# Kernel optimization log

Measured on AMD Instinct MI355X. Metric: run time of the kernel, lower is better.

## Reference

```python
import jax, jax.numpy as jnp
import numpy as np


def setup_inputs() -> dict:
    key = jax.random.key(0)
    k1, k2, k3 = jax.random.split(key, 3)
    B, K, C, H, W = 8, 8, 256, 64, 64
    return {
        "IR_features": jax.random.normal(k1, (B, K, C, H, W), dtype=jnp.float32),
        "CR_features": jax.random.normal(k2, (B, K, C, H, W), dtype=jnp.float32),
        "CT_feature": jax.random.normal(k3, (B, C, H, W), dtype=jnp.float32),
    }


def reference(IR_features, CR_features, CT_feature):
    # sim: [B, K, C, 1, 1] = <CT, CR>_{HW} / ||CR||_{HW}
    dot = jnp.sum(CT_feature[:, None] * CR_features, axis=(3, 4), keepdims=True)
    norm = jnp.sqrt(jnp.sum(CR_features ** 2, axis=(3, 4), keepdims=True))
    sim = dot / norm
    weights = jax.nn.softmax(sim * 2.0, axis=1)  # softmax over K styles
    # style feature: weighted sum over K -> [B, C, H, W]
    style_feature = jnp.sum(IR_features * weights, axis=1)
    return style_feature
```

## Files before the change

### kernel.cpp

```cpp
#include <hip/hip_runtime.h>
#include <math.h>

#define B_DIM 8
#define K_DIM 8
#define C_DIM 256
#define HW4   1024
#define CHUNK 4

__global__ __launch_bounds__(256)
void dfs_mixer_fused(const float4* __restrict__ IR,
                     const float4* __restrict__ CR,
                     const float4* __restrict__ CT,
                     float4* __restrict__ out)
{
    const int bid = blockIdx.x;
    const int b   = bid >> 8;
    const int c   = bid & 255;
    const int t   = threadIdx.x;

    const int ct_base = bid * HW4;

    float4 ct[CHUNK];
#pragma unroll
    for (int i = 0; i < CHUNK; ++i)
        ct[i] = CT[ct_base + i * 256 + t];

    float dot[K_DIM], ss[K_DIM];
#pragma unroll
    for (int k = 0; k < K_DIM; ++k) {
        const int cr_base = ((b * K_DIM + k) * C_DIM + c) * HW4;
        float d = 0.f, s = 0.f;
#pragma unroll
        for (int i = 0; i < CHUNK; ++i) {
            float4 cr = CR[cr_base + i * 256 + t];
            d += ct[i].x * cr.x + ct[i].y * cr.y + ct[i].z * cr.z + ct[i].w * cr.w;
            s += cr.x * cr.x + cr.y * cr.y + cr.z * cr.z + cr.w * cr.w;
        }
        dot[k] = d; ss[k] = s;
    }

#pragma unroll
    for (int k = 0; k < K_DIM; ++k) {
#pragma unroll
        for (int off = 32; off >= 1; off >>= 1) {
            dot[k] += __shfl_xor(dot[k], off, 64);
            ss[k]  += __shfl_xor(ss[k],  off, 64);
        }
    }

    __shared__ float red_d[4][K_DIM];
    __shared__ float red_s[4][K_DIM];
    __shared__ float wts[K_DIM];
    const int wave = t >> 6;
    const int lane = t & 63;
    if (lane == 0) {
#pragma unroll
        for (int k = 0; k < K_DIM; ++k) {
            red_d[wave][k] = dot[k];
            red_s[wave][k] = ss[k];
        }
    }
    __syncthreads();
    if (t == 0) {
        float sim[K_DIM];
        float m = -1e30f;
#pragma unroll
        for (int k = 0; k < K_DIM; ++k) {
            float d = red_d[0][k] + red_d[1][k] + red_d[2][k] + red_d[3][k];
            float s = red_s[0][k] + red_s[1][k] + red_s[2][k] + red_s[3][k];
            sim[k] = 2.0f * d / sqrtf(s);
            m = fmaxf(m, sim[k]);
        }
        float sum = 0.f;
#pragma unroll
        for (int k = 0; k < K_DIM; ++k) { sim[k] = expf(sim[k] - m); sum += sim[k]; }
        const float inv = 1.0f / sum;
#pragma unroll
        for (int k = 0; k < K_DIM; ++k) wts[k] = sim[k] * inv;
    }
    __syncthreads();

    float w[K_DIM];
#pragma unroll
    for (int k = 0; k < K_DIM; ++k) w[k] = wts[k];

#pragma unroll
    for (int i = 0; i < CHUNK; ++i) {
        float4 acc = make_float4(0.f, 0.f, 0.f, 0.f);
#pragma unroll
        for (int k = 0; k < K_DIM; ++k) {
            const int ir_base = ((b * K_DIM + k) * C_DIM + c) * HW4;
            float4 v = IR[ir_base + i * 256 + t];
            acc.x += w[k] * v.x;
            acc.y += w[k] * v.y;
            acc.z += w[k] * v.z;
            acc.w += w[k] * v.w;
        }
        out[ct_base + i * 256 + t] = acc;
    }
}

extern "C" void kernel_launch(void* const* d_in, const int* in_sizes, int n_in,
                              void* d_out, int out_size, void* d_ws, size_t ws_size,
                              hipStream_t stream) {
    const float4* IR = (const float4*)d_in[0];
    const float4* CR = (const float4*)d_in[1];
    const float4* CT = (const float4*)d_in[2];
    float4* out      = (float4*)d_out;

    dfs_mixer_fused<<<B_DIM * C_DIM, 256, 0, stream>>>(IR, CR, CT, out);
}
```

Measured before the change: 531.4 us.

## Use 1024-thread blocks with two waves per style for the reduction phase

Grows each block from 256 to 1024 threads. In the reduction phase each pair of waves handles one style k over the full plane, so every thread keeps a single dot/norm accumulator instead of eight. The weighted sum over K is reorganised so each thread produces one float4 output, and the softmax is spread across eight threads. This gives more memory parallelism per block and lower register pressure, but CT is now reloaded by each of the 8 style wave pairs and there are more block-wide barriers.

```diff
diff --git a/kernel.cpp b/kernel.cpp
--- a/kernel.cpp
+++ b/kernel.cpp
@@ -5,99 +5,84 @@
 #define K_DIM 8
 #define C_DIM 256
 #define HW4   1024
-#define CHUNK 4
 
-__global__ __launch_bounds__(256)
+__global__ __launch_bounds__(1024, 8)
 void dfs_mixer_fused(const float4* __restrict__ IR,
                      const float4* __restrict__ CR,
                      const float4* __restrict__ CT,
                      float4* __restrict__ out)
 {
-    const int bid = blockIdx.x;
-    const int b   = bid >> 8;
-    const int c   = bid & 255;
-    const int t   = threadIdx.x;
+    const int bid  = blockIdx.x;
+    const int b    = bid >> 8;
+    const int c    = bid & 255;
+    const int t    = threadIdx.x;
+    const int wave = t >> 6;
+    const int lane = t & 63;
 
     const int ct_base = bid * HW4;
 
-    float4 ct[CHUNK];
+    const int k  = wave >> 1;
+    const int li = ((wave & 1) << 6) | lane;
+    const int cr_base = (b * (K_DIM * C_DIM) + k * C_DIM + c) * HW4;
+
+    float d = 0.f, s = 0.f;
 #pragma unroll
-    for (int i = 0; i < CHUNK; ++i)
-        ct[i] = CT[ct_base + i * 256 + t];
-
-    float dot[K_DIM], ss[K_DIM];
-#pragma unroll
-    for (int k = 0; k < K_DIM; ++k) {
-        const int cr_base = ((b * K_DIM + k) * C_DIM + c) * HW4;
-        float d = 0.f, s = 0.f;
-#pragma unroll
-        for (int i = 0; i < CHUNK; ++i) {
-            float4 cr = CR[cr_base + i * 256 + t];
-            d += ct[i].x * cr.x + ct[i].y * cr.y + ct[i].z * cr.z + ct[i].w * cr.w;
-            s += cr.x * cr.x + cr.y * cr.y + cr.z * cr.z + cr.w * cr.w;
-        }
-        dot[k] = d; ss[k] = s;
+    for (int i = 0; i < 8; ++i) {
+        const int off = li + i * 128;
+        float4 ctv = CT[ct_base + off];
+        float4 crv = CR[cr_base + off];
+        d = fmaf(ctv.x, crv.x, d); d = fmaf(ctv.y, crv.y, d);
+        d = fmaf(ctv.z, crv.z, d); d = fmaf(ctv.w, crv.w, d);
+        s = fmaf(crv.x, crv.x, s); s = fmaf(crv.y, crv.y, s);
+        s = fmaf(crv.z, crv.z, s); s = fmaf(crv.w, crv.w, s);
     }
 
 #pragma unroll
-    for (int k = 0; k < K_DIM; ++k) {
-#pragma unroll
-        for (int off = 32; off >= 1; off >>= 1) {
-            dot[k] += __shfl_xor(dot[k], off, 64);
-            ss[k]  += __shfl_xor(ss[k],  off, 64);
-        }
+    for (int off = 32; off >= 1; off >>= 1) {
+        d += __shfl_xor(d, off, 64);
+        s += __shfl_xor(s, off, 64);
     }
 
-    __shared__ float red_d[4][K_DIM];
-    __shared__ float red_s[4][K_DIM];
+    __shared__ float red_d[16];
+    __shared__ float red_s[16];
+    __shared__ float simbuf[K_DIM];
     __shared__ float wts[K_DIM];
-    const int wave = t >> 6;
-    const int lane = t & 63;
-    if (lane == 0) {
-#pragma unroll
-        for (int k = 0; k < K_DIM; ++k) {
-            red_d[wave][k] = dot[k];
-            red_s[wave][k] = ss[k];
-        }
+    if (lane == 0) { red_d[wave] = d; red_s[wave] = s; }
+    __syncthreads();
+
+    if (t < K_DIM) {
+        float dd = red_d[2 * t] + red_d[2 * t + 1];
+        float ss = red_s[2 * t] + red_s[2 * t + 1];
+        simbuf[t] = 2.0f * dd / sqrtf(ss);
     }
     __syncthreads();
-    if (t == 0) {
-        float sim[K_DIM];
+
+    if (t < K_DIM) {
         float m = -1e30f;
 #pragma unroll
-        for (int k = 0; k < K_DIM; ++k) {
-            float d = red_d[0][k] + red_d[1][k] + red_d[2][k] + red_d[3][k];
-            float s = red_s[0][k] + red_s[1][k] + red_s[2][k] + red_s[3][k];
-            sim[k] = 2.0f * d / sqrtf(s);
-            m = fmaxf(m, sim[k]);
-        }
+        for (int j = 0; j < K_DIM; ++j) m = fmaxf(m, simbuf[j]);
         float sum = 0.f;
 #pragma unroll
-        for (int k = 0; k < K_DIM; ++k) { sim[k] = expf(sim[k] - m); sum += sim[k]; }
-        const float inv = 1.0f / sum;
-#pragma unroll
-        for (int k = 0; k < K_DIM; ++k) wts[k] = sim[k] * inv;
+        for (int j = 0; j < K_DIM; ++j) sum += expf(simbuf[j] - m);
+        wts[t] = expf(simbuf[t] - m) / sum;
     }
     __syncthreads();
 
     float w[K_DIM];
 #pragma unroll
-    for (int k = 0; k < K_DIM; ++k) w[k] = wts[k];
+    for (int j = 0; j < K_DIM; ++j) w[j] = wts[j];
 
+    const int plane0 = (b * (K_DIM * C_DIM) + c) * HW4 + t;
+    float4 acc = make_float4(0.f, 0.f, 0.f, 0.f);
 #pragma unroll
-    for (int i = 0; i < CHUNK; ++i) {
-        float4 acc = make_float4(0.f, 0.f, 0.f, 0.f);
-#pragma unroll
-        for (int k = 0; k < K_DIM; ++k) {
-            const int ir_base = ((b * K_DIM + k) * C_DIM + c) * HW4;
-            float4 v = IR[ir_base + i * 256 + t];
-            acc.x += w[k] * v.x;
-            acc.y += w[k] * v.y;
-            acc.z += w[k] * v.z;
-            acc.w += w[k] * v.w;
-        }
-        out[ct_base + i * 256 + t] = acc;
+    for (int j = 0; j < K_DIM; ++j) {
+        float4 v = IR[plane0 + j * (C_DIM * HW4)];
+        acc.x = fmaf(w[j], v.x, acc.x);
+        acc.y = fmaf(w[j], v.y, acc.y);
+        acc.z = fmaf(w[j], v.z, acc.z);
+        acc.w = fmaf(w[j], v.w, acc.w);
     }
+    out[ct_base + t] = acc;
 }
 
 extern "C" void kernel_launch(void* const* d_in, const int* in_sizes, int n_in,
@@ -108,5 +93,5 @@
     const float4* CT = (const float4*)d_in[2];
     float4* out      = (float4*)d_out;
 
-    dfs_mixer_fused<<<B_DIM * C_DIM, 256, 0, stream>>>(IR, CR, CT, out);
+    dfs_mixer_fused<<<B_DIM * C_DIM, 1024, 0, stream>>>(IR, CR, CT, out);
 }
```

Result: no change. 524.4 us (-1.3%).

## Split fused mixer into reduce, softmax, and mix kernels for more parallelism

Applied to the files above, without the earlier changes.

Replaces the single fused kernel, which ran one block per (b,c) and looped over K planes, with three kernels. The first reduces each (b,k,c) plane in its own block, the second computes the softmax weights per (b,c), and the third mixes IR with four blocks per (b,c). This raises block count and memory-level parallelism for a bandwidth-bound workload. In exchange it adds two extra launches, workspace traffic, and CT reads repeated once per k instead of being held in registers.

```diff
diff --git a/kernel.cpp b/kernel.cpp
--- a/kernel.cpp
+++ b/kernel.cpp
@@ -5,99 +5,106 @@
 #define K_DIM 8
 #define C_DIM 256
 #define HW4   1024
-#define CHUNK 4
+#define BC    (B_DIM * C_DIM)
+#define BKC   (B_DIM * K_DIM * C_DIM)
 
 __global__ __launch_bounds__(256)
-void dfs_mixer_fused(const float4* __restrict__ IR,
-                     const float4* __restrict__ CR,
-                     const float4* __restrict__ CT,
-                     float4* __restrict__ out)
+void dfs_reduce(const float4* __restrict__ CR,
+                const float4* __restrict__ CT,
+                float* __restrict__ ws_dot,
+                float* __restrict__ ws_ss)
 {
     const int bid = blockIdx.x;
-    const int b   = bid >> 8;
-    const int c   = bid & 255;
+    const int b   = bid >> 11;
+    const int kc  = bid & 2047;
+    const int c   = kc & 255;
     const int t   = threadIdx.x;
 
-    const int ct_base = bid * HW4;
+    const int cr_base = bid * HW4;
+    const int ct_base = (b * C_DIM + c) * HW4;
 
-    float4 ct[CHUNK];
+    float d = 0.f, s = 0.f;
 #pragma unroll
-    for (int i = 0; i < CHUNK; ++i)
-        ct[i] = CT[ct_base + i * 256 + t];
+    for (int i = 0; i < 4; ++i) {
+        const int off = t + i * 256;
+        float4 cr = CR[cr_base + off];
+        float4 ct = CT[ct_base + off];
+        d = fmaf(ct.x, cr.x, d); d = fmaf(ct.y, cr.y, d);
+        d = fmaf(ct.z, cr.z, d); d = fmaf(ct.w, cr.w, d);
+        s = fmaf(cr.x, cr.x, s); s = fmaf(cr.y, cr.y, s);
+        s = fmaf(cr.z, cr.z, s); s = fmaf(cr.w, cr.w, s);
+    }
+#pragma unroll
+    for (int off = 32; off >= 1; off >>= 1) {
+        d += __shfl_xor(d, off, 64);
+        s += __shfl_xor(s, off, 64);
+    }
+    __shared__ float rd[4], rs[4];
+    const int wave = t >> 6, lane = t & 63;
+    if (lane == 0) { rd[wave] = d; rs[wave] = s; }
+    __syncthreads();
+    if (t == 0) {
+        ws_dot[bid] = rd[0] + rd[1] + rd[2] + rd[3];
+        ws_ss[bid]  = rs[0] + rs[1] + rs[2] + rs[3];
+    }
+}
 
-    float dot[K_DIM], ss[K_DIM];
+__global__ __launch_bounds__(256)
+void dfs_softmax(const float* __restrict__ ws_dot,
+                 const float* __restrict__ ws_ss,
+                 float* __restrict__ ws_w)
+{
+    const int idx = blockIdx.x * 256 + threadIdx.x;
+    if (idx >= BC) return;
+    const int b = idx >> 8, c = idx & 255;
+
+    float sim[K_DIM];
+    float m = -1e30f;
 #pragma unroll
     for (int k = 0; k < K_DIM; ++k) {
-        const int cr_base = ((b * K_DIM + k) * C_DIM + c) * HW4;
-        float d = 0.f, s = 0.f;
+        const int p = (b * K_DIM + k) * C_DIM + c;
+        float dd = ws_dot[p];
+        float ss = ws_ss[p];
+        sim[k] = 2.0f * dd / sqrtf(ss);
+        m = fmaxf(m, sim[k]);
+    }
+    float sum = 0.f;
 #pragma unroll
-        for (int i = 0; i < CHUNK; ++i) {
-            float4 cr = CR[cr_base + i * 256 + t];
-            d += ct[i].x * cr.x + ct[i].y * cr.y + ct[i].z * cr.z + ct[i].w * cr.w;
-            s += cr.x * cr.x + cr.y * cr.y + cr.z * cr.z + cr.w * cr.w;
-        }
-        dot[k] = d; ss[k] = s;
-    }
+    for (int k = 0; k < K_DIM; ++k) { sim[k] = expf(sim[k] - m); sum += sim[k]; }
+    const float inv = 1.0f / sum;
+#pragma unroll
+    for (int k = 0; k < K_DIM; ++k)
+        ws_w[(b * K_DIM + k) * C_DIM + c] = sim[k] * inv;
+}
 
+__global__ __launch_bounds__(256)
+void dfs_mix(const float4* __restrict__ IR,
+             const float* __restrict__ ws_w,
+             float4* __restrict__ out)
+{
+    const int bid   = blockIdx.x;
+    const int q     = bid & 3;
+    const int bc    = bid >> 2;
+    const int b     = bc >> 8, c = bc & 255;
+    const int t     = threadIdx.x;
+    const int off   = q * 256 + t;
+
+    __shared__ float w[K_DIM];
+    if (t < K_DIM) w[t] = ws_w[(b * K_DIM + t) * C_DIM + c];
+    __syncthreads();
+
+    const int plane0 = (b * (K_DIM * C_DIM) + c) * HW4 + off;
+    float4 acc = make_float4(0.f, 0.f, 0.f, 0.f);
 #pragma unroll
     for (int k = 0; k < K_DIM; ++k) {
-#pragma unroll
-        for (int off = 32; off >= 1; off >>= 1) {
-            dot[k] += __shfl_xor(dot[k], off, 64);
-            ss[k]  += __shfl_xor(ss[k],  off, 64);
-        }
+        float4 v = IR[plane0 + k * (C_DIM * HW4)];
+        const float wk = w[k];
+        acc.x = fmaf(wk, v.x, acc.x);
+        acc.y = fmaf(wk, v.y, acc.y);
+        acc.z = fmaf(wk, v.z, acc.z);
+        acc.w = fmaf(wk, v.w, acc.w);
     }
-
-    __shared__ float red_d[4][K_DIM];
-    __shared__ float red_s[4][K_DIM];
-    __shared__ float wts[K_DIM];
-    const int wave = t >> 6;
-    const int lane = t & 63;
-    if (lane == 0) {
-#pragma unroll
-        for (int k = 0; k < K_DIM; ++k) {
-            red_d[wave][k] = dot[k];
-            red_s[wave][k] = ss[k];
-        }
-    }
-    __syncthreads();
-    if (t == 0) {
-        float sim[K_DIM];
-        float m = -1e30f;
-#pragma unroll
-        for (int k = 0; k < K_DIM; ++k) {
-            float d = red_d[0][k] + red_d[1][k] + red_d[2][k] + red_d[3][k];
-            float s = red_s[0][k] + red_s[1][k] + red_s[2][k] + red_s[3][k];
-            sim[k] = 2.0f * d / sqrtf(s);
-            m = fmaxf(m, sim[k]);
-        }
-        float sum = 0.f;
-#pragma unroll
-        for (int k = 0; k < K_DIM; ++k) { sim[k] = expf(sim[k] - m); sum += sim[k]; }
-        const float inv = 1.0f / sum;
-#pragma unroll
-        for (int k = 0; k < K_DIM; ++k) wts[k] = sim[k] * inv;
-    }
-    __syncthreads();
-
-    float w[K_DIM];
-#pragma unroll
-    for (int k = 0; k < K_DIM; ++k) w[k] = wts[k];
-
-#pragma unroll
-    for (int i = 0; i < CHUNK; ++i) {
-        float4 acc = make_float4(0.f, 0.f, 0.f, 0.f);
-#pragma unroll
-        for (int k = 0; k < K_DIM; ++k) {
-            const int ir_base = ((b * K_DIM + k) * C_DIM + c) * HW4;
-            float4 v = IR[ir_base + i * 256 + t];
-            acc.x += w[k] * v.x;
-            acc.y += w[k] * v.y;
-            acc.z += w[k] * v.z;
-            acc.w += w[k] * v.w;
-        }
-        out[ct_base + i * 256 + t] = acc;
-    }
+    out[bc * HW4 + off] = acc;
 }
 
 extern "C" void kernel_launch(void* const* d_in, const int* in_sizes, int n_in,
@@ -108,5 +115,11 @@
     const float4* CT = (const float4*)d_in[2];
     float4* out      = (float4*)d_out;
 
-    dfs_mixer_fused<<<B_DIM * C_DIM, 256, 0, stream>>>(IR, CR, CT, out);
+    float* ws_dot = (float*)d_ws;
+    float* ws_ss  = ws_dot + BKC;
+    float* ws_w   = ws_ss + BKC;
+
+    dfs_reduce <<<BKC,     256, 0, stream>>>(CR, CT, ws_dot, ws_ss);
+    dfs_softmax<<<BC / 256,256, 0, stream>>>(ws_dot, ws_ss, ws_w);
+    dfs_mix    <<<BC * 4,  256, 0, stream>>>(IR, ws_w, out);
 }
```

Result: no change. 535.8 us (+0.8%).
